# Kernel optimization log

Measured on AMD Instinct MI355X. Metric: run time of the kernel, lower is better.

Reference implementation:

```python
import jax, jax.numpy as jnp
import numpy as np
import math

# Constants derived from init kwargs
SAMPLE_RATE = 44100
ATTACK_S = 10.0 / 1000.0
RELEASE_S = 100.0 / 1000.0
GA = math.exp(-1.0 / (SAMPLE_RATE * ATTACK_S))   # attack coefficient
GR = math.exp(-1.0 / (SAMPLE_RATE * RELEASE_S))  # release coefficient
APPLY_RECTIFICATION = True


def setup_inputs() -> dict:
    key = jax.random.key(0)
    B, T, C = 32, 262144, 2
    signal = jax.random.normal(key, (B, T, C), dtype=jnp.float32)
    return {"signal": signal}


def reference(signal) -> jnp.ndarray:
    # signal: (B, T, C)
    x = jnp.abs(signal) if APPLY_RECTIFICATION else signal
    ga = jnp.asarray(GA, dtype=x.dtype)
    gr = jnp.asarray(GR, dtype=x.dtype)
    xs = jnp.transpose(x, (1, 0, 2))  # (T, B, C) so scan runs over time
    state0 = jnp.zeros(x.shape[0:1] + x.shape[2:3], dtype=x.dtype)  # (B, C)

    def step(state, x_t):
        attack = x_t > state
        new_state = jnp.where(attack,
                              (1.0 - ga) * x_t + ga * state,
                              (1.0 - gr) * x_t + gr * state)
        return new_state, new_state

    _, env = jax.lax.scan(step, state0, xs)  # env: (T, B, C)
    return jnp.transpose(env, (1, 0, 2))  # (B, T, C)
```

## Files before the change

### kernel.cpp

```cpp
#include <hip/hip_runtime.h>
#include <math.h>


#define TLEN   262144
#define CH     2
#define NCHUNK 256
#define LCHUNK (TLEN / NCHUNK)
#define WARM   7168
#define K      32
#define P2     36

#define GA_F 0.997734995305814f
#define GR_F 0.999773268339838f
#define CA_F (1.0f - GA_F)
#define KK_F ((1.0f - GR_F) / (1.0f - GA_F))
#define U0_F (1.275f / CA_F)

__device__ __forceinline__ void loadG(float4& b0, float4& b1, const float* __restrict__ in,
                                      int tg, int o0, int o1) {
  b0 = *reinterpret_cast<const float4*>(in + (tg * CH + o0));
  b1 = *reinterpret_cast<const float4*>(in + (tg * CH + o1));
}

__device__ __forceinline__ void writeL(float* __restrict__ Lb, const float4& b0,
                                       const float4& b1, int w0, int w1) {
  *reinterpret_cast<float2*>(Lb + w0)      = make_float2(b0.x, b0.z);
  *reinterpret_cast<float2*>(Lb + w0 + P2) = make_float2(b0.y, b0.w);
  *reinterpret_cast<float2*>(Lb + w1)      = make_float2(b1.x, b1.z);
  *reinterpret_cast<float2*>(Lb + w1 + P2) = make_float2(b1.y, b1.w);
}

__device__ __forceinline__ void readX(float4 (&xs)[8], const float* __restrict__ Lb, int r0) {
#pragma unroll
  for (int g = 0; g < 8; ++g)
    xs[g] = *reinterpret_cast<const float4*>(Lb + r0 + 4 * g);
}

__device__ __forceinline__ void scanT(const float4 (&xs)[8], float& u, float4 (&o)[8]) {
#pragma unroll
  for (int g = 0; g < 8; ++g) {
    float x;
    x = xs[g].x; u = fmaxf(fmaf(GA_F, u, fabsf(x)), fmaf(GR_F, u, KK_F * fabsf(x))); o[g].x = u;
    x = xs[g].y; u = fmaxf(fmaf(GA_F, u, fabsf(x)), fmaf(GR_F, u, KK_F * fabsf(x))); o[g].y = u;
    x = xs[g].z; u = fmaxf(fmaf(GA_F, u, fabsf(x)), fmaf(GR_F, u, KK_F * fabsf(x))); o[g].z = u;
    x = xs[g].w; u = fmaxf(fmaf(GA_F, u, fabsf(x)), fmaf(GR_F, u, KK_F * fabsf(x))); o[g].w = u;
  }
}

__device__ __forceinline__ void storeT(float* __restrict__ out, const float* __restrict__ Lout,
                                       int tg, int o0, int o1, int w0, int w1) {
  float2 lo, hi;
  lo = *reinterpret_cast<const float2*>(Lout + w0);
  hi = *reinterpret_cast<const float2*>(Lout + w0 + P2);
  *reinterpret_cast<float4*>(out + (tg * CH + o0)) =
      make_float4(lo.x * CA_F, hi.x * CA_F, lo.y * CA_F, hi.y * CA_F);
  lo = *reinterpret_cast<const float2*>(Lout + w1);
  hi = *reinterpret_cast<const float2*>(Lout + w1 + P2);
  *reinterpret_cast<float4*>(out + (tg * CH + o1)) =
      make_float4(lo.x * CA_F, hi.x * CA_F, lo.y * CA_F, hi.y * CA_F);
}

__global__ __launch_bounds__(256, 1)
void EnvelopeFollower_30245159698452_kernel(const float* __restrict__ in,
                                            float* __restrict__ out) {
  __shared__ float L[3][64 * P2];
  __shared__ float Lout[64 * P2];

  const int bid   = blockIdx.x;
  const int chunk = (bid & 7) * (NCHUNK / 8) + (bid >> 3);
  const int tid   = threadIdx.x;
  const int lane  = tid & 63;
  const int wid   = tid >> 6;
  const int r     = tid >> 4;
  const int c     = tid & 15;

  const int o0 = (r * TLEN + 2 * c) * CH;
  const int o1 = ((r + 16) * TLEN + 2 * c) * CH;
  const int w0 = (2 * r) * P2 + 2 * c;
  const int w1 = w0 + 32 * P2;

  const int  ch  = (wid << 4) | (lane & 15);
  const int  r0  = ch * P2;
  float* LoutRow = Lout + r0;
  const bool wlo = (lane & 48) == 0;

  const int t0     = chunk * LCHUNK;
  const int ts     = (t0 >= WARM) ? (t0 - WARM) : 0;
  const int nt_raw = (t0 + LCHUNK - ts) >> 5;
  const int nt     = nt_raw + ((6 - (nt_raw % 6)) % 6);
  const int nw     = (t0 - ts) >> 5;

  float u = (ts == 0) ? 0.0f : (float)U0_F;

  float4 A0, A1, C0, C1, xs[8], o[8];

  loadG(A0, A1, in, ts + 0 * K, o0, o1);
  loadG(C0, C1, in, ts + 1 * K, o0, o1);
  writeL(L[0], A0, A1, w0, w1);
  writeL(L[1], C0, C1, w0, w1);
  loadG(A0, A1, in, ts + 2 * K, o0, o1);
  loadG(C0, C1, in, ts + 3 * K, o0, o1);
  __syncthreads();
  readX(xs, L[0], r0);

#define PH(IDX, LW, B0_, B1_, LR)                                            \
  {                                                                          \
    const int idx_ = (IDX);                                                  \
    __syncthreads();                                                         \
    writeL(LW, B0_, B1_, w0, w1);                                            \
    { int tg = ts + (idx_ + 4) * K;                                          \
      tg = (tg > TLEN - K) ? (TLEN - K) : tg;                                \
      loadG(B0_, B1_, in, tg, o0, o1); }                                     \
    scanT(xs, u, o);                                                         \
    const bool outp = (idx_ >= nw) && (idx_ < nt_raw);                       \
    if (outp && wlo) {                                                       \
      _Pragma("unroll")                                                      \
      for (int g = 0; g < 8; ++g)                                            \
        *reinterpret_cast<float4*>(LoutRow + 4 * g) = o[g];                  \
    }                                                                        \
    if (outp) {                                                              \
      __syncthreads();                                                       \
      storeT(out, Lout, ts + idx_ * K, o0, o1, w0, w1);                      \
    }                                                                        \
    readX(xs, LR, r0);                                                       \
  }

  for (int i = 0; i < nt; i += 6) {
    PH(i + 0, L[2], A0, A1, L[1])
    PH(i + 1, L[0], C0, C1, L[2])
    PH(i + 2, L[1], A0, A1, L[0])
    PH(i + 3, L[2], C0, C1, L[1])
    PH(i + 4, L[0], A0, A1, L[2])
    PH(i + 5, L[1], C0, C1, L[0])
  }
}

extern "C" void kernel_launch(void* const* d_in, const int* in_sizes, int n_in,
                              void* d_out, int out_size, void* d_ws, size_t ws_size,
                              hipStream_t stream) {
  const float* in = (const float*)d_in[0];
  float* out = (float*)d_out;
  hipLaunchKernelGGL(EnvelopeFollower_30245159698452_kernel,
                     dim3(NCHUNK), dim3(256), 0, stream, in, out);
}
```

Measured before the change: 141.9 us.

## Dual-chain scan per lane, swizzled LDS, lgkm-only barriers, shorter warmup

Each lane now runs two independent envelope recurrences (channels k and k+32) instead of one chain replicated across lane groups. LDS writes and reads use an XOR swizzle to avoid bank conflicts. __syncthreads is replaced by explicit s_waitcnt lgkmcnt plus s_barrier, so in-flight global prefetches are not drained at every phase. The warmup length is cut from 7168 to 6144 samples, which reduces redundant work. The risk is that the warmup is no longer long enough to converge from the U0 estimate, and that the hand-written barriers may order LDS accesses incorrectly.

```diff
diff --git a/kernel.cpp b/kernel.cpp
--- a/kernel.cpp
+++ b/kernel.cpp
@@ -6,7 +6,7 @@
 #define CH     2
 #define NCHUNK 256
 #define LCHUNK (TLEN / NCHUNK)
-#define WARM   7168
+#define WARM   6144
 #define K      32
 #define P2     36
 
@@ -30,35 +30,46 @@
   *reinterpret_cast<float2*>(Lb + w1 + P2) = make_float2(b1.y, b1.w);
 }
 
-__device__ __forceinline__ void readX(float4 (&xs)[8], const float* __restrict__ Lb, int r0) {
+__device__ __forceinline__ void readX(float4 (&xs)[8], const float* __restrict__ Lb,
+                                      int rbase, const int (&rcol)[8]) {
 #pragma unroll
   for (int g = 0; g < 8; ++g)
-    xs[g] = *reinterpret_cast<const float4*>(Lb + r0 + 4 * g);
+    xs[g] = *reinterpret_cast<const float4*>(Lb + rbase + rcol[g]);
 }
 
-__device__ __forceinline__ void scanT(const float4 (&xs)[8], float& u, float4 (&o)[8]) {
+__device__ __forceinline__ void scanT(const float4 (&xa)[8], const float4 (&xb)[8],
+                                      float& uA, float& uB,
+                                      float4 (&oa)[8], float4 (&ob)[8]) {
 #pragma unroll
   for (int g = 0; g < 8; ++g) {
-    float x;
-    x = xs[g].x; u = fmaxf(fmaf(GA_F, u, fabsf(x)), fmaf(GR_F, u, KK_F * fabsf(x))); o[g].x = u;
-    x = xs[g].y; u = fmaxf(fmaf(GA_F, u, fabsf(x)), fmaf(GR_F, u, KK_F * fabsf(x))); o[g].y = u;
-    x = xs[g].z; u = fmaxf(fmaf(GA_F, u, fabsf(x)), fmaf(GR_F, u, KK_F * fabsf(x))); o[g].z = u;
-    x = xs[g].w; u = fmaxf(fmaf(GA_F, u, fabsf(x)), fmaf(GR_F, u, KK_F * fabsf(x))); o[g].w = u;
+    float xA, xB;
+#define SSTEP(CMP)                                                               \
+    xA = xa[g].CMP; xB = xb[g].CMP;                                              \
+    uA = fmaxf(fmaf(GA_F, uA, fabsf(xA)), fmaf(GR_F, uA, KK_F * fabsf(xA)));     \
+    uB = fmaxf(fmaf(GA_F, uB, fabsf(xB)), fmaf(GR_F, uB, KK_F * fabsf(xB)));     \
+    oa[g].CMP = uA; ob[g].CMP = uB;
+    SSTEP(x) SSTEP(y) SSTEP(z) SSTEP(w)
+#undef SSTEP
   }
 }
 
 __device__ __forceinline__ void storeT(float* __restrict__ out, const float* __restrict__ Lout,
-                                       int tg, int o0, int o1, int w0, int w1) {
+                                       int tg, int o0, int o1, int q0, int q1) {
   float2 lo, hi;
-  lo = *reinterpret_cast<const float2*>(Lout + w0);
-  hi = *reinterpret_cast<const float2*>(Lout + w0 + P2);
+  lo = *reinterpret_cast<const float2*>(Lout + q0);
+  hi = *reinterpret_cast<const float2*>(Lout + q0 + P2);
   *reinterpret_cast<float4*>(out + (tg * CH + o0)) =
       make_float4(lo.x * CA_F, hi.x * CA_F, lo.y * CA_F, hi.y * CA_F);
-  lo = *reinterpret_cast<const float2*>(Lout + w1);
-  hi = *reinterpret_cast<const float2*>(Lout + w1 + P2);
+  lo = *reinterpret_cast<const float2*>(Lout + q1);
+  hi = *reinterpret_cast<const float2*>(Lout + q1 + P2);
   *reinterpret_cast<float4*>(out + (tg * CH + o1)) =
       make_float4(lo.x * CA_F, hi.x * CA_F, lo.y * CA_F, hi.y * CA_F);
 }
+
+#define LGKM_BAR(N)                                           \
+  asm volatile("s_waitcnt lgkmcnt(" #N ")" ::: "memory");     \
+  __builtin_amdgcn_s_barrier();                               \
+  __builtin_amdgcn_sched_barrier(0);
 
 __global__ __launch_bounds__(256, 1)
 void EnvelopeFollower_30245159698452_kernel(const float* __restrict__ in,
@@ -71,18 +82,26 @@
   const int tid   = threadIdx.x;
   const int lane  = tid & 63;
   const int wid   = tid >> 6;
-  const int r     = tid >> 4;
+  const int r_    = tid >> 4;
   const int c     = tid & 15;
 
-  const int o0 = (r * TLEN + 2 * c) * CH;
-  const int o1 = ((r + 16) * TLEN + 2 * c) * CH;
-  const int w0 = (2 * r) * P2 + 2 * c;
-  const int w1 = w0 + 32 * P2;
+  const int o0 = (r_ * TLEN + 2 * c) * CH;
+  const int o1 = ((r_ + 16) * TLEN + 2 * c) * CH;
 
-  const int  ch  = (wid << 4) | (lane & 15);
-  const int  r0  = ch * P2;
-  float* LoutRow = Lout + r0;
-  const bool wlo = (lane & 48) == 0;
+  const int swzW = ((r_ >> 2) & 3) << 2;
+  const int w0   = (2 * r_) * P2 + ((2 * c) ^ swzW);
+  const int w1   = w0 + 32 * P2;
+
+  const int kA     = lane & 31;
+  const int swzR   = ((kA >> 3) & 3) << 2;
+  const int rbaseA = kA * P2;
+  const int rbaseB = (kA + 32) * P2;
+  int rcol[8];
+#pragma unroll
+  for (int g = 0; g < 8; ++g) rcol[g] = (4 * g) ^ swzR;
+
+  const int q0 = (2 * r_) * P2 + 2 * c;
+  const int q1 = q0 + 32 * P2;
 
   const int t0     = chunk * LCHUNK;
   const int ts     = (t0 >= WARM) ? (t0 - WARM) : 0;
@@ -90,9 +109,10 @@
   const int nt     = nt_raw + ((6 - (nt_raw % 6)) % 6);
   const int nw     = (t0 - ts) >> 5;
 
-  float u = (ts == 0) ? 0.0f : (float)U0_F;
+  float uA = (ts == 0) ? 0.0f : (float)U0_F;
+  float uB = uA;
 
-  float4 A0, A1, C0, C1, xs[8], o[8];
+  float4 A0, A1, C0, C1, xa[8], xb[8], oa[8], ob[8];
 
   loadG(A0, A1, in, ts + 0 * K, o0, o1);
   loadG(C0, C1, in, ts + 1 * K, o0, o1);
@@ -100,29 +120,37 @@
   writeL(L[1], C0, C1, w0, w1);
   loadG(A0, A1, in, ts + 2 * K, o0, o1);
   loadG(C0, C1, in, ts + 3 * K, o0, o1);
-  __syncthreads();
-  readX(xs, L[0], r0);
+  LGKM_BAR(0)
+  readX(xa, L[0], rbaseA, rcol);
+  readX(xb, L[0], rbaseB, rcol);
 
 #define PH(IDX, LW, B0_, B1_, LR)                                            \
   {                                                                          \
     const int idx_ = (IDX);                                                  \
-    __syncthreads();                                                         \
     writeL(LW, B0_, B1_, w0, w1);                                            \
     { int tg = ts + (idx_ + 4) * K;                                          \
       tg = (tg > TLEN - K) ? (TLEN - K) : tg;                                \
       loadG(B0_, B1_, in, tg, o0, o1); }                                     \
-    scanT(xs, u, o);                                                         \
-    const bool outp = (idx_ >= nw) && (idx_ < nt_raw);                       \
-    if (outp && wlo) {                                                       \
-      _Pragma("unroll")                                                      \
-      for (int g = 0; g < 8; ++g)                                            \
-        *reinterpret_cast<float4*>(LoutRow + 4 * g) = o[g];                  \
+    scanT(xa, xb, uA, uB, oa, ob);                                           \
+    if ((idx_ >= nw) && (idx_ < nt_raw)) {                                   \
+      if ((lane >> 4) == (wid & 1)) {           \
+        float* lrow = Lout + ((wid >= 2) ? (kA + 32) : kA) * P2;             \
+        if (wid >= 2) {                                                      \
+          _Pragma("unroll")                                                  \
+          for (int g = 0; g < 8; ++g)                                        \
+            *reinterpret_cast<float4*>(lrow + 4 * g) = ob[g];                \
+        } else {                                                             \
+          _Pragma("unroll")                                                  \
+          for (int g = 0; g < 8; ++g)                                        \
+            *reinterpret_cast<float4*>(lrow + 4 * g) = oa[g];                \
+        }                                                                    \
+      }                                                                      \
+      LGKM_BAR(0)                                                            \
+      storeT(out, Lout, ts + idx_ * K, o0, o1, q0, q1);                      \
     }                                                                        \
-    if (outp) {                                                              \
-      __syncthreads();                                                       \
-      storeT(out, Lout, ts + idx_ * K, o0, o1, w0, w1);                      \
-    }                                                                        \
-    readX(xs, LR, r0);                                                       \
+    readX(xa, LR, rbaseA, rcol);                                             \
+    readX(xb, LR, rbaseB, rcol);                                             \
+    LGKM_BAR(15)    \
   }
 
   for (int i = 0; i < nt; i += 6) {
```

New measurement: 210.2 us. 48.2% more time.

## Double time tile to 64, use 512 threads, shorten warmup, simplify buffering

Applied to the files above, without the earlier changes.

Raises the per-step time tile from 32 to 64 samples and the block to 512 threads. The LDS staging moves from a triple buffer to a double buffer, and the global load/store mapping changes so each thread touches one row with a contiguous 128-element span. The warmup window shrinks from 7168 to 6144 samples, which cuts redundant sequential scan work per chunk. The risks are a smaller warmup error margin, longer per-thread serial chains with more registers, and only 8 of 64 lanes per wave doing the scan.

```diff
diff --git a/kernel.cpp b/kernel.cpp
--- a/kernel.cpp
+++ b/kernel.cpp
@@ -6,9 +6,9 @@
 #define CH     2
 #define NCHUNK 256
 #define LCHUNK (TLEN / NCHUNK)
-#define WARM   7168
-#define K      32
-#define P2     36
+#define WARM   6144
+#define K      64
+#define P2     68
 
 #define GA_F 0.997734995305814f
 #define GR_F 0.999773268339838f
@@ -16,29 +16,30 @@
 #define KK_F ((1.0f - GR_F) / (1.0f - GA_F))
 #define U0_F (1.275f / CA_F)
 
-__device__ __forceinline__ void loadG(float4& b0, float4& b1, const float* __restrict__ in,
-                                      int tg, int o0, int o1) {
-  b0 = *reinterpret_cast<const float4*>(in + (tg * CH + o0));
-  b1 = *reinterpret_cast<const float4*>(in + (tg * CH + o1));
+__device__ __forceinline__ void loadG(float4 (&B)[2], const float* __restrict__ in,
+                                      int tg, int gof) {
+  B[0] = *reinterpret_cast<const float4*>(in + tg * CH + gof);
+  B[1] = *reinterpret_cast<const float4*>(in + tg * CH + gof + 64);
 }
 
-__device__ __forceinline__ void writeL(float* __restrict__ Lb, const float4& b0,
-                                       const float4& b1, int w0, int w1) {
-  *reinterpret_cast<float2*>(Lb + w0)      = make_float2(b0.x, b0.z);
-  *reinterpret_cast<float2*>(Lb + w0 + P2) = make_float2(b0.y, b0.w);
-  *reinterpret_cast<float2*>(Lb + w1)      = make_float2(b1.x, b1.z);
-  *reinterpret_cast<float2*>(Lb + w1 + P2) = make_float2(b1.y, b1.w);
+__device__ __forceinline__ void writeL(float* __restrict__ Lb, const float4 (&B)[2],
+                                       int w00, int w01) {
+  *reinterpret_cast<float2*>(Lb + w00)      = make_float2(B[0].x, B[0].z);
+  *reinterpret_cast<float2*>(Lb + w01)      = make_float2(B[0].y, B[0].w);
+  *reinterpret_cast<float2*>(Lb + w00 + 32) = make_float2(B[1].x, B[1].z);
+  *reinterpret_cast<float2*>(Lb + w01 + 32) = make_float2(B[1].y, B[1].w);
 }
 
-__device__ __forceinline__ void readX(float4 (&xs)[8], const float* __restrict__ Lb, int r0) {
+__device__ __forceinline__ void readX(float4 (&xs)[16], const float* __restrict__ Lb,
+                                      int rbase) {
 #pragma unroll
-  for (int g = 0; g < 8; ++g)
-    xs[g] = *reinterpret_cast<const float4*>(Lb + r0 + 4 * g);
+  for (int g = 0; g < 16; ++g)
+    xs[g] = *reinterpret_cast<const float4*>(Lb + rbase + 4 * g);
 }
 
-__device__ __forceinline__ void scanT(const float4 (&xs)[8], float& u, float4 (&o)[8]) {
+__device__ __forceinline__ void scanT(const float4 (&xs)[16], float& u, float4 (&o)[16]) {
 #pragma unroll
-  for (int g = 0; g < 8; ++g) {
+  for (int g = 0; g < 16; ++g) {
     float x;
     x = xs[g].x; u = fmaxf(fmaf(GA_F, u, fabsf(x)), fmaf(GR_F, u, KK_F * fabsf(x))); o[g].x = u;
     x = xs[g].y; u = fmaxf(fmaf(GA_F, u, fabsf(x)), fmaf(GR_F, u, KK_F * fabsf(x))); o[g].y = u;
@@ -48,22 +49,22 @@
 }
 
 __device__ __forceinline__ void storeT(float* __restrict__ out, const float* __restrict__ Lout,
-                                       int tg, int o0, int o1, int w0, int w1) {
+                                       int tg, int gof, int w00, int w01) {
   float2 lo, hi;
-  lo = *reinterpret_cast<const float2*>(Lout + w0);
-  hi = *reinterpret_cast<const float2*>(Lout + w0 + P2);
-  *reinterpret_cast<float4*>(out + (tg * CH + o0)) =
+  lo = *reinterpret_cast<const float2*>(Lout + w00);
+  hi = *reinterpret_cast<const float2*>(Lout + w01);
+  *reinterpret_cast<float4*>(out + tg * CH + gof) =
       make_float4(lo.x * CA_F, hi.x * CA_F, lo.y * CA_F, hi.y * CA_F);
-  lo = *reinterpret_cast<const float2*>(Lout + w1);
-  hi = *reinterpret_cast<const float2*>(Lout + w1 + P2);
-  *reinterpret_cast<float4*>(out + (tg * CH + o1)) =
+  lo = *reinterpret_cast<const float2*>(Lout + w00 + 32);
+  hi = *reinterpret_cast<const float2*>(Lout + w01 + 32);
+  *reinterpret_cast<float4*>(out + tg * CH + gof + 64) =
       make_float4(lo.x * CA_F, hi.x * CA_F, lo.y * CA_F, hi.y * CA_F);
 }
 
-__global__ __launch_bounds__(256, 1)
+__global__ __launch_bounds__(512, 1)
 void EnvelopeFollower_30245159698452_kernel(const float* __restrict__ in,
                                             float* __restrict__ out) {
-  __shared__ float L[3][64 * P2];
+  __shared__ float L[2][64 * P2];
   __shared__ float Lout[64 * P2];
 
   const int bid   = blockIdx.x;
@@ -71,67 +72,55 @@
   const int tid   = threadIdx.x;
   const int lane  = tid & 63;
   const int wid   = tid >> 6;
-  const int r     = tid >> 4;
+  const int r_    = tid >> 4;
   const int c     = tid & 15;
 
-  const int o0 = (r * TLEN + 2 * c) * CH;
-  const int o1 = ((r + 16) * TLEN + 2 * c) * CH;
-  const int w0 = (2 * r) * P2 + 2 * c;
-  const int w1 = w0 + 32 * P2;
+  const int gof = r_ * TLEN * CH + 4 * c;
+  const int w00 = (2 * r_) * P2 + 2 * c;
+  const int w01 = w00 + P2;
 
-  const int  ch  = (wid << 4) | (lane & 15);
-  const int  r0  = ch * P2;
-  float* LoutRow = Lout + r0;
-  const bool wlo = (lane & 48) == 0;
+  const int chainId = 8 * wid + (lane & 7);
+  const int rbase   = chainId * P2;
+  const bool writer = (lane < 8);
 
-  const int t0     = chunk * LCHUNK;
-  const int ts     = (t0 >= WARM) ? (t0 - WARM) : 0;
-  const int nt_raw = (t0 + LCHUNK - ts) >> 5;
-  const int nt     = nt_raw + ((6 - (nt_raw % 6)) % 6);
-  const int nw     = (t0 - ts) >> 5;
+  const int t0 = chunk * LCHUNK;
+  const int ts = (t0 >= WARM) ? (t0 - WARM) : 0;
+  const int nt = (t0 + LCHUNK - ts) >> 6;
+  const int nw = (t0 - ts) >> 6;
 
   float u = (ts == 0) ? 0.0f : (float)U0_F;
 
-  float4 A0, A1, C0, C1, xs[8], o[8];
+  float4 B[2], D[2], xs[16], o[16];
 
-  loadG(A0, A1, in, ts + 0 * K, o0, o1);
-  loadG(C0, C1, in, ts + 1 * K, o0, o1);
-  writeL(L[0], A0, A1, w0, w1);
-  writeL(L[1], C0, C1, w0, w1);
-  loadG(A0, A1, in, ts + 2 * K, o0, o1);
-  loadG(C0, C1, in, ts + 3 * K, o0, o1);
+  loadG(D, in, ts, gof);
+  writeL(L[0], D, w00, w01);
+  loadG(B, in, ts + K, gof);
   __syncthreads();
-  readX(xs, L[0], r0);
 
-#define PH(IDX, LW, B0_, B1_, LR)                                            \
+#define PH(IDX, LCUR, LNXT, BCUR, BNXT)                                      \
   {                                                                          \
     const int idx_ = (IDX);                                                  \
+    readX(xs, LCUR, rbase);                                                  \
+    { int tg = ts + (idx_ + 2) * K;                                          \
+      tg = (tg > TLEN - K) ? (TLEN - K) : tg;                                \
+      loadG(BNXT, in, tg, gof); }                                            \
+    writeL(LNXT, BCUR, w00, w01);                                            \
+    scanT(xs, u, o);                                                         \
+    if (idx_ >= nw) {                                                        \
+      if (writer) {                                                          \
+        _Pragma("unroll")                                                    \
+        for (int g = 0; g < 16; ++g)                                         \
+          *reinterpret_cast<float4*>(Lout + rbase + 4 * g) = o[g];           \
+      }                                                                      \
+      __syncthreads();                                                       \
+      storeT(out, Lout, ts + idx_ * K, gof, w00, w01);                       \
+    }                                                                        \
     __syncthreads();                                                         \
-    writeL(LW, B0_, B1_, w0, w1);                                            \
-    { int tg = ts + (idx_ + 4) * K;                                          \
-      tg = (tg > TLEN - K) ? (TLEN - K) : tg;                                \
-      loadG(B0_, B1_, in, tg, o0, o1); }                                     \
-    scanT(xs, u, o);                                                         \
-    const bool outp = (idx_ >= nw) && (idx_ < nt_raw);                       \
-    if (outp && wlo) {                                                       \
-      _Pragma("unroll")                                                      \
-      for (int g = 0; g < 8; ++g)                                            \
-        *reinterpret_cast<float4*>(LoutRow + 4 * g) = o[g];                  \
-    }                                                                        \
-    if (outp) {                                                              \
-      __syncthreads();                                                       \
-      storeT(out, Lout, ts + idx_ * K, o0, o1, w0, w1);                      \
-    }                                                                        \
-    readX(xs, LR, r0);                                                       \
   }
 
-  for (int i = 0; i < nt; i += 6) {
-    PH(i + 0, L[2], A0, A1, L[1])
-    PH(i + 1, L[0], C0, C1, L[2])
-    PH(i + 2, L[1], A0, A1, L[0])
-    PH(i + 3, L[2], C0, C1, L[1])
-    PH(i + 4, L[0], A0, A1, L[2])
-    PH(i + 5, L[1], C0, C1, L[0])
+  for (int i = 0; i < nt; i += 2) {
+    PH(i + 0, L[0], L[1], B, D)
+    PH(i + 1, L[1], L[0], D, B)
   }
 }
 
@@ -141,5 +130,5 @@
   const float* in = (const float*)d_in[0];
   float* out = (float*)d_out;
   hipLaunchKernelGGL(EnvelopeFollower_30245159698452_kernel,
-                     dim3(NCHUNK), dim3(256), 0, stream, in, out);
+                     dim3(NCHUNK), dim3(512), 0, stream, in, out);
 }
```

New measurement: 126.9 us. 1.12x faster.
